# Performance work log

Measured on AMD Instinct MI355X. Metric: run time of the kernel, lower is better.

The kernel has to match this reference:

```python
import jax, jax.numpy as jnp
import numpy as np

B, N = 2, 8192
D_POINTS, D_MODEL, K = 64, 128, 16


def _lin(key, fi, fo):
    return jax.random.normal(key, (fi, fo), jnp.float32) / np.sqrt(fi)


def setup_inputs() -> dict:
    key = jax.random.key(0)
    ks = jax.random.split(key, 16)
    return {
        "xyz": jax.random.normal(ks[0], (B, N, 3), jnp.float32),
        "normals": jax.random.normal(ks[1], (B, N, 3), jnp.float32),
        "features": jax.random.normal(ks[2], (B, N, D_POINTS), jnp.float32),
        "fc1_w": _lin(ks[3], D_POINTS, D_MODEL), "fc1_b": jnp.zeros((D_MODEL,), jnp.float32),
        "fc2_w": _lin(ks[4], D_MODEL, D_POINTS), "fc2_b": jnp.zeros((D_POINTS,), jnp.float32),
        "gamma_w1": _lin(ks[5], D_MODEL, D_MODEL), "gamma_b1": jnp.zeros((D_MODEL,), jnp.float32),
        "gamma_w2": _lin(ks[6], D_MODEL, D_MODEL), "gamma_b2": jnp.zeros((D_MODEL,), jnp.float32),
        "delta_w1": _lin(ks[7], 3, D_MODEL), "delta_b1": jnp.zeros((D_MODEL,), jnp.float32),
        "delta_w2": _lin(ks[8], D_MODEL, D_MODEL), "delta_b2": jnp.zeros((D_MODEL,), jnp.float32),
        "wq": _lin(ks[9], D_MODEL, D_MODEL),
        "wk": _lin(ks[10], D_MODEL, D_MODEL),
        "wv": _lin(ks[11], D_MODEL, D_MODEL),
    }


def _gather(points, idx):
    # points: (b, n, c), idx: (b, n, k) -> (b, n, k, c)
    b, n, c = points.shape
    k = idx.shape[-1]
    flat = jnp.take_along_axis(points, idx.reshape(b, n * k, 1), axis=1)
    return flat.reshape(b, n, k, c)


def reference(xyz, normals, features, fc1_w, fc1_b, fc2_w, fc2_b,
              gamma_w1, gamma_b1, gamma_w2, gamma_b2,
              delta_w1, delta_b1, delta_w2, delta_b2, wq, wk, wv):
    # pairwise squared distances (b, n, n)
    sq = jnp.sum(xyz * xyz, axis=-1)
    dists = sq[:, :, None] + sq[:, None, :] - 2.0 * jnp.einsum('bnd,bmd->bnm', xyz, xyz)
    _, knn_idx = jax.lax.top_k(-dists, K)  # k smallest distances (includes self)

    knn_xyz = _gather(xyz, knn_idx)                      # (b, n, k, 3)
    x = features @ fc1_w + fc1_b                         # (b, n, d_model)
    q = x @ wq                                           # (b, n, d_model)
    k_nbr = _gather(x @ wk, knn_idx)                     # (b, n, k, d_model)
    v_nbr = _gather(x @ wv, knn_idx)                     # (b, n, k, d_model)

    # positional encoding: fc_delta(rel_pos), ends with ReLU
    rel = xyz[:, :, None, :] - knn_xyz                   # (b, n, k, 3)
    pos_enc = jax.nn.relu(jax.nn.relu(rel @ delta_w1 + delta_b1) @ delta_w2 + delta_b2)

    # vector attention logits: fc_gamma(q - k + pos_enc)
    h = q[:, :, None, :] - k_nbr + pos_enc
    logits = jax.nn.relu(h @ gamma_w1 + gamma_b1) @ gamma_w2 + gamma_b2
    attn = jax.nn.softmax(logits / np.sqrt(D_MODEL), axis=-2)  # softmax over neighbors

    res = jnp.einsum('bnkf,bnkf->bnf', attn, v_nbr + pos_enc)
    res = res @ fc2_w + fc2_b + features
    return res, attn
```

## Files before the change

### kernel.cpp

```cpp
#include <hip/hip_runtime.h>
#include <cstdint>

typedef unsigned long long ull;
typedef __bf16 bf16x8 __attribute__((ext_vector_type(8)));
typedef float f32x4 __attribute__((ext_vector_type(4)));
typedef float f32x2 __attribute__((ext_vector_type(2)));

#define NPTS 8192
#define NB 2
#define KNN 16
#define DM 128
#define PADK 136

__device__ __forceinline__ float sq3f(float x, float y, float z) {
    return __fadd_rn(__fadd_rn(__fmul_rn(x, x), __fmul_rn(y, y)), __fmul_rn(z, z));
}
__device__ __forceinline__ unsigned ford(unsigned u) {
    return (u & 0x80000000u) ? ~u : (u | 0x80000000u);
}
__device__ __forceinline__ float inv_ford(unsigned f) {
    unsigned u = (f & 0x80000000u) ? (f ^ 0x80000000u) : ~f;
    return __uint_as_float(u);
}
__device__ __forceinline__ f32x2 pk_mul(f32x2 a, f32x2 b) {
    f32x2 d;
    asm("v_pk_mul_f32 %0, %1, %2" : "=v"(d) : "v"(a), "v"(b));
    return d;
}
__device__ __forceinline__ f32x2 pk_add(f32x2 a, f32x2 b) {
    f32x2 d;
    asm("v_pk_add_f32 %0, %1, %2" : "=v"(d) : "v"(a), "v"(b));
    return d;
}

__device__ __forceinline__ void knn_body(const float* __restrict__ xyz,
                                         int* __restrict__ idx_out,
                                         char* lds, int bid) {
    float4* xsA = (float4*)lds;
    float4* xsB = (float4*)(lds + 8192);
    const int t = threadIdx.x;
    const int wv = t >> 6, lane = t & 63;
    const int q_id = bid * 4 + wv;
    const int b = q_id >> 13;
    const int i = q_id & (NPTS - 1);
    const float* xb = xyz + (size_t)b * NPTS * 3;
    const float qx = xb[3 * i + 0], qy = xb[3 * i + 1], qz = xb[3 * i + 2];
    const float sqi = sq3f(qx, qy, qz);
    const f32x2 qx2 = {qx, qx}, qy2 = {qy, qy}, qz2 = {qz, qz};
    const f32x2 sqi2 = {sqi, sqi}, ntwo2 = {-2.0f, -2.0f};

    unsigned list_hi = 0xffffffffu, list_lo = 0xffffffffu;
    float thrF = __uint_as_float(0x7f800000u);

#define INSERT(FC, CKLO)                                                                 \
    {                                                                                    \
        unsigned ck_hi = ford(__float_as_uint(FC));                                      \
        unsigned ck_lo = (CKLO);                                                         \
        unsigned ph = __shfl_up(list_hi, 1);                                             \
        unsigned pl = __shfl_up(list_lo, 1);                                             \
        bool lt = (ck_hi < list_hi) || (ck_hi == list_hi && ck_lo < list_lo);            \
        bool ge = (lane == 0) || (ck_hi > ph) || (ck_hi == ph && ck_lo >= pl);           \
        list_hi = lt ? (ge ? ck_hi : ph) : list_hi;                                      \
        list_lo = lt ? (ge ? ck_lo : pl) : list_lo;                                      \
        unsigned th = (unsigned)__builtin_amdgcn_readlane((int)list_hi, 15);             \
        th = (th > 0xff800000u) ? 0xff800000u : th;            \
        thrF = fminf(thrF, inv_ford(th));                                                \
    }

    for (int ch = 0; ch < 8; ++ch) {
        __syncthreads();
#pragma unroll
        for (int e = 0; e < 2; e++) {
            int s = t + e * 256;
            int c0 = ((s >> 6) << 7) + (s & 63);
            int g = ch * 1024 + c0;
            float x0 = xb[3 * g + 0], y0 = xb[3 * g + 1], z0 = xb[3 * g + 2];
            float x1 = xb[3 * (g + 64) + 0], y1 = xb[3 * (g + 64) + 1], z1 = xb[3 * (g + 64) + 2];
            xsA[s] = make_float4(x0, x1, y0, y1);
            xsB[s] = make_float4(z0, z1, sq3f(x0, y0, z0), sq3f(x1, y1, z1));
        }
        __syncthreads();
        for (int m = 0; m < 8; m++) {
            const int s = m * 64 + lane;
            float4 A = xsA[s];
            float4 B = xsB[s];
            f32x2 ax = {A.x, A.y}, ay = {A.z, A.w};
            f32x2 bz = {B.x, B.y}, bs = {B.z, B.w};
            f32x2 p1 = pk_mul(qx2, ax);
            f32x2 p2 = pk_mul(qy2, ay);
            f32x2 p3 = pk_mul(qz2, bz);
            f32x2 s1 = pk_add(p1, p2);
            f32x2 s2 = pk_add(s1, p3);
            f32x2 num = pk_add(sqi2, bs);
            f32x2 tm = pk_mul(ntwo2, s2);
            f32x2 dd = pk_add(num, tm);
            float dA = dd.x, dB = dd.y;
            if (ch == 0 && m == 0) {
                float mn = fminf(dA, dB);
                mn = fminf(mn, __shfl_xor(mn, 1));
                mn = fminf(mn, __shfl_xor(mn, 2));
                float mx = mn;
                mx = fmaxf(mx, __shfl_xor(mx, 4));
                mx = fmaxf(mx, __shfl_xor(mx, 8));
                mx = fmaxf(mx, __shfl_xor(mx, 16));
                mx = fmaxf(mx, __shfl_xor(mx, 32));
                thrF = mx;
            }
            ull balA = __ballot(dA <= thrF);
            ull balB = __ballot(dB <= thrF);
            if ((balA | balB) == 0ull) continue;
            const unsigned jbase = (unsigned)(ch * 1024 + m * 128);
            while (balA) {
                int l = (int)__builtin_ctzll(balA);
                balA &= balA - 1;
                float fc = __uint_as_float(
                    (unsigned)__builtin_amdgcn_readlane(__float_as_int(dA), l));
                if (fc <= thrF) INSERT(fc, jbase + (unsigned)l)
            }
            while (balB) {
                int l = (int)__builtin_ctzll(balB);
                balB &= balB - 1;
                float fc = __uint_as_float(
                    (unsigned)__builtin_amdgcn_readlane(__float_as_int(dB), l));
                if (fc <= thrF) INSERT(fc, jbase + 64u + (unsigned)l)
            }
        }
    }
#undef INSERT
    if (lane < 16)
        idx_out[q_id * 16 + lane] = (int)list_lo;
}

__device__ __forceinline__ void xqkv_body(const float* __restrict__ feats,
                                          const float* __restrict__ fc1_w,
                                          const float* __restrict__ fc1_b,
                                          const __bf16* __restrict__ wqt,
                                          const __bf16* __restrict__ wkt,
                                          const __bf16* __restrict__ wvt,
                                          float* __restrict__ qo,
                                          float* __restrict__ kko,
                                          float* __restrict__ vvo,
                                          char* lds, int bid) {
    float* At = (float*)lds;
    __bf16* Ab = (__bf16*)lds;
    const int t = threadIdx.x;
    const int base = bid * 64;

#pragma unroll
    for (int e = 0; e < 16; e++) {
        int id = t + e * 256;
        int r = id >> 6, c = id & 63;
        At[c * 65 + r] = feats[(size_t)(base + r) * 64 + c];
    }
    __syncthreads();
    const int r0 = (t >> 4) * 4;
    const int c0 = (t & 15) * 8;
    float acc[4][8];
#pragma unroll
    for (int i = 0; i < 4; i++)
#pragma unroll
        for (int j = 0; j < 8; j++) acc[i][j] = fc1_b[c0 + j];
#pragma unroll 4
    for (int kk = 0; kk < 64; ++kk) {
        float a0 = At[kk * 65 + r0 + 0];
        float a1 = At[kk * 65 + r0 + 1];
        float a2 = At[kk * 65 + r0 + 2];
        float a3 = At[kk * 65 + r0 + 3];
        const float4 w0 = *(const float4*)&fc1_w[kk * 128 + c0];
        const float4 w1 = *(const float4*)&fc1_w[kk * 128 + c0 + 4];
        float wj[8] = {w0.x, w0.y, w0.z, w0.w, w1.x, w1.y, w1.z, w1.w};
#pragma unroll
        for (int j = 0; j < 8; j++) {
            acc[0][j] += a0 * wj[j];
            acc[1][j] += a1 * wj[j];
            acc[2][j] += a2 * wj[j];
            acc[3][j] += a3 * wj[j];
        }
    }
    __syncthreads();

#pragma unroll
    for (int i = 0; i < 4; i++)
#pragma unroll
        for (int j = 0; j < 8; j++)
            Ab[(r0 + i) * PADK + c0 + j] = (__bf16)acc[i][j];
    __syncthreads();

    const int lane = t & 63;
    const int lr = lane & 15, lg = lane >> 4;
    const int rbase = (t >> 6) * 16;

#define QGEMM(WPTR, OUT)                                                                   \
    {                                                                                      \
        f32x4 accg[8];                                                                     \
        _Pragma("unroll")                                                                  \
        for (int ct = 0; ct < 8; ct++) accg[ct] = (f32x4){0.f, 0.f, 0.f, 0.f};             \
        _Pragma("unroll")                                                                  \
        for (int kt = 0; kt < 4; kt++) {                                                   \
            const int ko = kt * 32 + 8 * lg;                                               \
            bf16x8 a0 = *(const bf16x8*)&Ab[(rbase + lr) * PADK + ko];                     \
            _Pragma("unroll")                                                              \
            for (int ct = 0; ct < 8; ct++) {                                               \
                bf16x8 bv = *(const bf16x8*)&WPTR[(ct * 16 + lr) * 128 + ko];              \
                accg[ct] = __builtin_amdgcn_mfma_f32_16x16x32_bf16(a0, bv, accg[ct], 0, 0, 0); \
            }                                                                              \
        }                                                                                  \
        _Pragma("unroll")                                                                  \
        for (int ct = 0; ct < 8; ct++)                                                     \
            _Pragma("unroll")                                                              \
            for (int e = 0; e < 4; e++)                                                    \
                OUT[(size_t)(base + rbase + 4 * lg + e) * 128 + ct * 16 + lr] = accg[ct][e]; \
    }

    QGEMM(wqt, qo)
    QGEMM(wkt, kko)
    QGEMM(wvt, vvo)
#undef QGEMM
}

__global__ __launch_bounds__(256, 6) void mega_kernel(const float* __restrict__ xyz,
                                                      int* __restrict__ idxw,
                                                      const float* __restrict__ feats,
                                                      const float* __restrict__ fc1_w,
                                                      const float* __restrict__ fc1_b,
                                                      const __bf16* __restrict__ wqt,
                                                      const __bf16* __restrict__ wkt,
                                                      const __bf16* __restrict__ wvt,
                                                      float* __restrict__ qo,
                                                      float* __restrict__ kko,
                                                      float* __restrict__ vvo) {
    __shared__ __align__(16) char lds[17408];
    if (blockIdx.x < 256)
        xqkv_body(feats, fc1_w, fc1_b, wqt, wkt, wvt, qo, kko, vvo, lds, blockIdx.x);
    else
        knn_body(xyz, idxw, lds, blockIdx.x - 256);
}

__global__ __launch_bounds__(256) void wprep_kernel(const float* __restrict__ d2,
                                                    const float* __restrict__ g1,
                                                    const float* __restrict__ g2,
                                                    const float* __restrict__ wq,
                                                    const float* __restrict__ wk,
                                                    const float* __restrict__ wv,
                                                    __bf16* __restrict__ d2t,
                                                    __bf16* __restrict__ g1t,
                                                    __bf16* __restrict__ g2t,
                                                    __bf16* __restrict__ wqt,
                                                    __bf16* __restrict__ wkt,
                                                    __bf16* __restrict__ wvt) {
    const int bi = blockIdx.x;
    const float* src = (bi == 0) ? d2 : (bi == 1) ? g1 : (bi == 2) ? g2
                     : (bi == 3) ? wq : (bi == 4) ? wk : wv;
    __bf16* dst = (bi == 0) ? d2t : (bi == 1) ? g1t : (bi == 2) ? g2t
                : (bi == 3) ? wqt : (bi == 4) ? wkt : wvt;
#pragma unroll
    for (int e = 0; e < 64; e++) {
        int id = threadIdx.x + e * 256;
        int k = id >> 7, n = id & 127;
        dst[n * 128 + k] = (__bf16)src[id];
    }
}

#define STAGE_W(SRC)                                                                       \
    {                                                                                      \
        _Pragma("unroll")                                                                  \
        for (int e = 0; e < 8; e++) {                                                      \
            int ch = t + e * 256;                                                          \
            int r = ch >> 4, ck = ch & 15;                                                 \
            *(bf16x8*)&Wb[r * PADK + ck * 8] = *(const bf16x8*)&SRC[r * 128 + ck * 8];     \
        }                                                                                  \
    }

#define DO_GEMM(ACC0, ACC1, WPTR)                                                          \
    {                                                                                      \
        _Pragma("unroll")                                                                  \
        for (int kt = 0; kt < 4; kt++) {                                                   \
            const int ko = kt * 32 + 8 * lg;                                               \
            bf16x8 a0 = *(const bf16x8*)&Ab[(rbase + lr) * PADK + ko];                     \
            bf16x8 a1 = *(const bf16x8*)&Ab[(rbase + 16 + lr) * PADK + ko];                \
            _Pragma("unroll")                                                              \
            for (int ct = 0; ct < 8; ct++) {                                               \
                bf16x8 bv = *(const bf16x8*)&WPTR[(ct * 16 + lr) * PADK + ko];             \
                ACC0[ct] = __builtin_amdgcn_mfma_f32_16x16x32_bf16(a0, bv, ACC0[ct], 0, 0, 0); \
                ACC1[ct] = __builtin_amdgcn_mfma_f32_16x16x32_bf16(a1, bv, ACC1[ct], 0, 0, 0); \
            }                                                                              \
        }                                                                                  \
    }

__global__ __launch_bounds__(256, 2) void k345_kernel(const float* __restrict__ xyz,
                                                      const int* __restrict__ idxw,
                                                      const float* __restrict__ q,
                                                      const float* __restrict__ xk,
                                                      const float* __restrict__ xv,
                                                      const float* __restrict__ d1,
                                                      const float* __restrict__ bd1,
                                                      const float* __restrict__ bd2,
                                                      const float* __restrict__ bg1,
                                                      const float* __restrict__ bg2,
                                                      const __bf16* __restrict__ d2t,
                                                      const __bf16* __restrict__ g1t,
                                                      const __bf16* __restrict__ g2t,
                                                      float* __restrict__ attn,
                                                      float* __restrict__ res_pre) {
    __shared__ __bf16 Ab[128 * PADK];
    __shared__ __bf16 Wb[128 * PADK];
    __shared__ float rels[128 * 4];
    __shared__ int jrow[128];
    __shared__ float d1s[3 * 128];
    __shared__ float bd1s[128], bd2s[128], bg1s[128], bg2s[128];

    const int t = threadIdx.x;
    const int wv = t >> 6;
    const int lane = t & 63;
    const int lr = lane & 15, lg = lane >> 4;
    const int R0 = blockIdx.x * 128;
    const int b = R0 >> 17;
    const int rbase = wv * 32;

#pragma unroll
    for (int e = 0; e < 2; e++) { int id = t + e * 256; if (id < 384) d1s[id] = d1[id]; }
    if (t < 128) {
        bd1s[t] = bd1[t]; bd2s[t] = bd2[t]; bg1s[t] = bg1[t]; bg2s[t] = bg2[t];
    } else {
        int r = t - 128;
        int j = idxw[R0 + r];
        jrow[r] = j;
        const float* pn = xyz + (size_t)((R0 + r) >> 4) * 3;
        const float* pj = xyz + (size_t)((b << 13) + j) * 3;
        rels[r * 4 + 0] = pn[0] - pj[0];
        rels[r * 4 + 1] = pn[1] - pj[1];
        rels[r * 4 + 2] = pn[2] - pj[2];
    }
    STAGE_W(d2t)
    __syncthreads();

    {
        const int c = t & 127;
        const float w0 = d1s[c], w1 = d1s[128 + c], w2 = d1s[256 + c], bb = bd1s[c];
#pragma unroll
        for (int e = 0; e < 64; e++) {
            int r = (t >> 7) + e * 2;
            float v = fmaf(rels[r * 4 + 2], w2,
                      fmaf(rels[r * 4 + 1], w1, fmaf(rels[r * 4 + 0], w0, bb)));
            Ab[r * PADK + c] = (__bf16)fmaxf(v, 0.0f);
        }
    }
    __syncthreads();

    f32x4 acc0[8], acc1[8];
#pragma unroll
    for (int ct = 0; ct < 8; ct++) {
        float bb = bd2s[ct * 16 + lr];
        acc0[ct] = (f32x4){bb, bb, bb, bb};
        acc1[ct] = acc0[ct];
    }
    DO_GEMM(acc0, acc1, Wb)
    f32x4 pos0[8], pos1[8];
#pragma unroll
    for (int ct = 0; ct < 8; ct++) {
#pragma unroll
        for (int e = 0; e < 4; e++) {
            pos0[ct][e] = fmaxf(acc0[ct][e], 0.0f);
            pos1[ct][e] = fmaxf(acc1[ct][e], 0.0f);
        }
    }

#pragma unroll
    for (int rt = 0; rt < 2; rt++) {
        const int rloc = rbase + rt * 16 + 4 * lg;
        const size_t qbase = (size_t)((R0 + rloc) >> 4) * 128;
        const int j0 = jrow[rloc + 0], j1 = jrow[rloc + 1];
        const int j2 = jrow[rloc + 2], j3 = jrow[rloc + 3];
        const size_t kb0 = (size_t)((b << 13) + j0) * 128;
        const size_t kb1 = (size_t)((b << 13) + j1) * 128;
        const size_t kb2 = (size_t)((b << 13) + j2) * 128;
        const size_t kb3 = (size_t)((b << 13) + j3) * 128;
        f32x4* posR = rt ? pos1 : pos0;
#pragma unroll
        for (int ct = 0; ct < 8; ct++) {
            const int c = ct * 16 + lr;
            const float qv = q[qbase + c];
            f32x4 p = posR[ct];
            Ab[(rloc + 0) * PADK + c] = (__bf16)(p[0] + qv - xk[kb0 + c]);
            Ab[(rloc + 1) * PADK + c] = (__bf16)(p[1] + qv - xk[kb1 + c]);
            Ab[(rloc + 2) * PADK + c] = (__bf16)(p[2] + qv - xk[kb2 + c]);
            Ab[(rloc + 3) * PADK + c] = (__bf16)(p[3] + qv - xk[kb3 + c]);
        }
    }
    __syncthreads();
    STAGE_W(g1t)
    __syncthreads();

#pragma unroll
    for (int ct = 0; ct < 8; ct++) {
        float bb = bg1s[ct * 16 + lr];
        acc0[ct] = (f32x4){bb, bb, bb, bb};
        acc1[ct] = acc0[ct];
    }
    DO_GEMM(acc0, acc1, Wb)
#pragma unroll
    for (int rt = 0; rt < 2; rt++) {
        const int rloc = rbase + rt * 16 + 4 * lg;
        f32x4* accR = rt ? acc1 : acc0;
#pragma unroll
        for (int ct = 0; ct < 8; ct++) {
            const int c = ct * 16 + lr;
            f32x4 p = accR[ct];
            Ab[(rloc + 0) * PADK + c] = (__bf16)fmaxf(p[0], 0.0f);
            Ab[(rloc + 1) * PADK + c] = (__bf16)fmaxf(p[1], 0.0f);
            Ab[(rloc + 2) * PADK + c] = (__bf16)fmaxf(p[2], 0.0f);
            Ab[(rloc + 3) * PADK + c] = (__bf16)fmaxf(p[3], 0.0f);
        }
    }
    __syncthreads();
    STAGE_W(g2t)
    __syncthreads();

#pragma unroll
    for (int ct = 0; ct < 8; ct++) {
        float bb = bg2s[ct * 16 + lr];
        acc0[ct] = (f32x4){bb, bb, bb, bb};
        acc1[ct] = acc0[ct];
    }
    DO_GEMM(acc0, acc1, Wb)
    const float scale = 0.08838834764831845f;
#pragma unroll
    for (int rt = 0; rt < 2; rt++) {
        const int rloc = rbase + rt * 16 + 4 * lg;
        const int j0 = jrow[rloc + 0], j1 = jrow[rloc + 1];
        const int j2 = jrow[rloc + 2], j3 = jrow[rloc + 3];
        const size_t vb0 = (size_t)((b << 13) + j0) * 128;
        const size_t vb1 = (size_t)((b << 13) + j1) * 128;
        const size_t vb2 = (size_t)((b << 13) + j2) * 128;
        const size_t vb3 = (size_t)((b << 13) + j3) * 128;
        f32x4* accR = rt ? acc1 : acc0;
        f32x4* posR = rt ? pos1 : pos0;
#pragma unroll
        for (int ct = 0; ct < 8; ct++) {
            const int c = ct * 16 + lr;
            f32x4 p = accR[ct];
            float l0 = p[0] * scale, l1 = p[1] * scale, l2 = p[2] * scale, l3 = p[3] * scale;
            float m = fmaxf(fmaxf(l0, l1), fmaxf(l2, l3));
            m = fmaxf(m, __shfl_xor(m, 16));
            m = fmaxf(m, __shfl_xor(m, 32));
            float e0 = __expf(l0 - m), e1 = __expf(l1 - m);
            float e2 = __expf(l2 - m), e3 = __expf(l3 - m);
            float s = (e0 + e1) + (e2 + e3);
            s += __shfl_xor(s, 16);
            s += __shfl_xor(s, 32);
            float inv = 1.0f / s;
            float a0 = e0 * inv, a1 = e1 * inv, a2 = e2 * inv, a3 = e3 * inv;
            size_t ob = (size_t)(R0 + rloc) * 128 + c;
            attn[ob + 0 * 128] = a0;
            attn[ob + 1 * 128] = a1;
            attn[ob + 2 * 128] = a2;
            attn[ob + 3 * 128] = a3;
            f32x4 pp = posR[ct];
            float r = a0 * (xv[vb0 + c] + pp[0])
                    + a1 * (xv[vb1 + c] + pp[1])
                    + a2 * (xv[vb2 + c] + pp[2])
                    + a3 * (xv[vb3 + c] + pp[3]);
            r += __shfl_xor(r, 16);
            r += __shfl_xor(r, 32);
            if (lg == 0)
                res_pre[(size_t)((R0 >> 4) + wv * 2 + rt) * 128 + c] = r;
        }
    }
}

__global__ __launch_bounds__(256, 1) void k6_kernel(const float* __restrict__ res_pre,
                                                    const float* __restrict__ w,
                                                    const float* __restrict__ bias,
                                                    const float* __restrict__ feats,
                                                    float* __restrict__ res_out) {
    __shared__ float At[128 * 65];
    __shared__ __align__(16) float Wt[128 * 64];
    const int t = threadIdx.x;
    const int base = blockIdx.x * 64;
#pragma unroll
    for (int e = 0; e < 32; e++) {
        int id = t + e * 256;
        int r = id >> 7, c = id & 127;
        At[c * 65 + r] = res_pre[(size_t)(base + r) * 128 + c];
    }
#pragma unroll
    for (int e = 0; e < 32; e++) { int id = t + e * 256; Wt[id] = w[id]; }
    __syncthreads();
    const int r0 = (t >> 4) * 4;
    const int c0 = (t & 15) * 4;
    float acc[4][4];
#pragma unroll
    for (int i = 0; i < 4; i++)
#pragma unroll
        for (int j = 0; j < 4; j++) acc[i][j] = bias[c0 + j];
#pragma unroll 4
    for (int kk = 0; kk < 128; ++kk) {
        float a0 = At[kk * 65 + r0 + 0];
        float a1 = At[kk * 65 + r0 + 1];
        float a2 = At[kk * 65 + r0 + 2];
        float a3 = At[kk * 65 + r0 + 3];
        const float4 w0 = *(const float4*)&Wt[kk * 64 + c0];
        float wj[4] = {w0.x, w0.y, w0.z, w0.w};
#pragma unroll
        for (int j = 0; j < 4; j++) {
            acc[0][j] += a0 * wj[j];
            acc[1][j] += a1 * wj[j];
            acc[2][j] += a2 * wj[j];
            acc[3][j] += a3 * wj[j];
        }
    }
#pragma unroll
    for (int i = 0; i < 4; i++)
#pragma unroll
        for (int j = 0; j < 4; j++)
            res_out[(size_t)(base + r0 + i) * 64 + c0 + j] =
                acc[i][j] + feats[(size_t)(base + r0 + i) * 64 + c0 + j];
}

extern "C" void kernel_launch(void* const* d_in, const int* in_sizes, int n_in,
                              void* d_out, int out_size, void* d_ws, size_t ws_size,
                              hipStream_t stream) {
    (void)in_sizes; (void)n_in; (void)out_size; (void)ws_size;
    const float* xyz   = (const float*)d_in[0];
    const float* feats = (const float*)d_in[2];
    const float* fc1_w = (const float*)d_in[3];
    const float* fc1_b = (const float*)d_in[4];
    const float* fc2_w = (const float*)d_in[5];
    const float* fc2_b = (const float*)d_in[6];
    const float* g1    = (const float*)d_in[7];
    const float* bg1   = (const float*)d_in[8];
    const float* g2    = (const float*)d_in[9];
    const float* bg2   = (const float*)d_in[10];
    const float* d1    = (const float*)d_in[11];
    const float* bd1   = (const float*)d_in[12];
    const float* d2    = (const float*)d_in[13];
    const float* bd2   = (const float*)d_in[14];
    const float* wq    = (const float*)d_in[15];
    const float* wk    = (const float*)d_in[16];
    const float* wv    = (const float*)d_in[17];

    int* idxw   = (int*)d_ws;
    float* qbuf = (float*)((char*)d_ws + (1 << 20));
    float* kbuf = qbuf + 2097152;
    float* vbuf = kbuf + 2097152;
    float* rpre = vbuf + 2097152;
    __bf16* d2t = (__bf16*)(rpre + 2097152);
    __bf16* g1t = d2t + 16384;
    __bf16* g2t = g1t + 16384;
    __bf16* wqt = g2t + 16384;
    __bf16* wkt = wqt + 16384;
    __bf16* wvt = wkt + 16384;

    float* res_out = (float*)d_out;
    float* attn    = res_out + 1048576;

    wprep_kernel<<<6, 256, 0, stream>>>(d2, g1, g2, wq, wk, wv,
                                        d2t, g1t, g2t, wqt, wkt, wvt);
    mega_kernel<<<4352, 256, 0, stream>>>(xyz, idxw, feats, fc1_w, fc1_b,
                                          wqt, wkt, wvt, qbuf, kbuf, vbuf);
    k345_kernel<<<2048, 256, 0, stream>>>(xyz, idxw, qbuf, kbuf, vbuf, d1, bd1, bd2, bg1, bg2,
                                          d2t, g1t, g2t, attn, rpre);
    k6_kernel<<<256, 256, 0, stream>>>(rpre, fc2_w, fc2_b, feats, res_out);
}
```

Baseline: 247.9 us.

## Fuse fc2 into attention kernel, read weights from global, interleave knn/qkv blocks

The final fc2 projection kernel is removed. Each attention block now computes its 8 output rows of fc2 plus residual directly from an LDS buffer, which drops the res_pre round trip and one launch. The MFMA GEMMs read bf16 weight fragments straight from global/L2 instead of staging them into a padded LDS buffer. That frees LDS and lets occupancy rise to 3 blocks per CU, at the cost of unpadded global reads. The mega kernel also interleaves one qkv block per 16 knn blocks so the two workloads mix across CUs instead of running in sequence.

```diff
diff --git a/kernel.cpp b/kernel.cpp
--- a/kernel.cpp
+++ b/kernel.cpp
@@ -230,10 +230,12 @@
                                                       float* __restrict__ kko,
                                                       float* __restrict__ vvo) {
     __shared__ __align__(16) char lds[17408];
-    if (blockIdx.x < 256)
-        xqkv_body(feats, fc1_w, fc1_b, wqt, wkt, wvt, qo, kko, vvo, lds, blockIdx.x);
+    const int g = blockIdx.x / 17;
+    const int p = blockIdx.x % 17;
+    if (p == 0)
+        xqkv_body(feats, fc1_w, fc1_b, wqt, wkt, wvt, qo, kko, vvo, lds, g);
     else
-        knn_body(xyz, idxw, lds, blockIdx.x - 256);
+        knn_body(xyz, idxw, lds, g * 16 + (p - 1));
 }
 
 __global__ __launch_bounds__(256) void wprep_kernel(const float* __restrict__ d2,
@@ -261,17 +263,7 @@
     }
 }
 
-#define STAGE_W(SRC)                                                                       \
-    {                                                                                      \
-        _Pragma("unroll")                                                                  \
-        for (int e = 0; e < 8; e++) {                                                      \
-            int ch = t + e * 256;                                                          \
-            int r = ch >> 4, ck = ch & 15;                                                 \
-            *(bf16x8*)&Wb[r * PADK + ck * 8] = *(const bf16x8*)&SRC[r * 128 + ck * 8];     \
-        }                                                                                  \
-    }
-
-#define DO_GEMM(ACC0, ACC1, WPTR)                                                          \
+#define DO_GEMM_G(ACC0, ACC1, WPTR)                                                        \
     {                                                                                      \
         _Pragma("unroll")                                                                  \
         for (int kt = 0; kt < 4; kt++) {                                                   \
@@ -280,14 +272,14 @@
             bf16x8 a1 = *(const bf16x8*)&Ab[(rbase + 16 + lr) * PADK + ko];                \
             _Pragma("unroll")                                                              \
             for (int ct = 0; ct < 8; ct++) {                                               \
-                bf16x8 bv = *(const bf16x8*)&WPTR[(ct * 16 + lr) * PADK + ko];             \
+                bf16x8 bv = *(const bf16x8*)&WPTR[(ct * 16 + lr) * 128 + ko];              \
                 ACC0[ct] = __builtin_amdgcn_mfma_f32_16x16x32_bf16(a0, bv, ACC0[ct], 0, 0, 0); \
                 ACC1[ct] = __builtin_amdgcn_mfma_f32_16x16x32_bf16(a1, bv, ACC1[ct], 0, 0, 0); \
             }                                                                              \
         }                                                                                  \
     }
 
-__global__ __launch_bounds__(256, 2) void k345_kernel(const float* __restrict__ xyz,
+__global__ __launch_bounds__(256, 3) void k345_kernel(const float* __restrict__ xyz,
                                                       const int* __restrict__ idxw,
                                                       const float* __restrict__ q,
                                                       const float* __restrict__ xk,
@@ -300,10 +292,13 @@
                                                       const __bf16* __restrict__ d2t,
                                                       const __bf16* __restrict__ g1t,
                                                       const __bf16* __restrict__ g2t,
+                                                      const float* __restrict__ feats,
+                                                      const float* __restrict__ fc2,
+                                                      const float* __restrict__ fc2_b,
                                                       float* __restrict__ attn,
-                                                      float* __restrict__ res_pre) {
+                                                      float* __restrict__ res_out) {
     __shared__ __bf16 Ab[128 * PADK];
-    __shared__ __bf16 Wb[128 * PADK];
+    __shared__ float rpre_s[8][128];
     __shared__ float rels[128 * 4];
     __shared__ int jrow[128];
     __shared__ float d1s[3 * 128];
@@ -331,7 +326,6 @@
         rels[r * 4 + 1] = pn[1] - pj[1];
         rels[r * 4 + 2] = pn[2] - pj[2];
     }
-    STAGE_W(d2t)
     __syncthreads();
 
     {
@@ -354,7 +348,7 @@
         acc0[ct] = (f32x4){bb, bb, bb, bb};
         acc1[ct] = acc0[ct];
     }
-    DO_GEMM(acc0, acc1, Wb)
+    DO_GEMM_G(acc0, acc1, d2t)
     f32x4 pos0[8], pos1[8];
 #pragma unroll
     for (int ct = 0; ct < 8; ct++) {
@@ -388,8 +382,6 @@
         }
     }
     __syncthreads();
-    STAGE_W(g1t)
-    __syncthreads();
 
 #pragma unroll
     for (int ct = 0; ct < 8; ct++) {
@@ -397,7 +389,8 @@
         acc0[ct] = (f32x4){bb, bb, bb, bb};
         acc1[ct] = acc0[ct];
     }
-    DO_GEMM(acc0, acc1, Wb)
+    DO_GEMM_G(acc0, acc1, g1t)
+    __syncthreads();
 #pragma unroll
     for (int rt = 0; rt < 2; rt++) {
         const int rloc = rbase + rt * 16 + 4 * lg;
@@ -413,8 +406,6 @@
         }
     }
     __syncthreads();
-    STAGE_W(g2t)
-    __syncthreads();
 
 #pragma unroll
     for (int ct = 0; ct < 8; ct++) {
@@ -422,7 +413,7 @@
         acc0[ct] = (f32x4){bb, bb, bb, bb};
         acc1[ct] = acc0[ct];
     }
-    DO_GEMM(acc0, acc1, Wb)
+    DO_GEMM_G(acc0, acc1, g2t)
     const float scale = 0.08838834764831845f;
 #pragma unroll
     for (int rt = 0; rt < 2; rt++) {
@@ -463,58 +454,26 @@
             r += __shfl_xor(r, 16);
             r += __shfl_xor(r, 32);
             if (lg == 0)
-                res_pre[(size_t)((R0 >> 4) + wv * 2 + rt) * 128 + c] = r;
-        }
-    }
-}
-
-__global__ __launch_bounds__(256, 1) void k6_kernel(const float* __restrict__ res_pre,
-                                                    const float* __restrict__ w,
-                                                    const float* __restrict__ bias,
-                                                    const float* __restrict__ feats,
-                                                    float* __restrict__ res_out) {
-    __shared__ float At[128 * 65];
-    __shared__ __align__(16) float Wt[128 * 64];
-    const int t = threadIdx.x;
-    const int base = blockIdx.x * 64;
-#pragma unroll
-    for (int e = 0; e < 32; e++) {
-        int id = t + e * 256;
-        int r = id >> 7, c = id & 127;
-        At[c * 65 + r] = res_pre[(size_t)(base + r) * 128 + c];
-    }
-#pragma unroll
-    for (int e = 0; e < 32; e++) { int id = t + e * 256; Wt[id] = w[id]; }
-    __syncthreads();
-    const int r0 = (t >> 4) * 4;
-    const int c0 = (t & 15) * 4;
-    float acc[4][4];
-#pragma unroll
-    for (int i = 0; i < 4; i++)
-#pragma unroll
-        for (int j = 0; j < 4; j++) acc[i][j] = bias[c0 + j];
-#pragma unroll 4
-    for (int kk = 0; kk < 128; ++kk) {
-        float a0 = At[kk * 65 + r0 + 0];
-        float a1 = At[kk * 65 + r0 + 1];
-        float a2 = At[kk * 65 + r0 + 2];
-        float a3 = At[kk * 65 + r0 + 3];
-        const float4 w0 = *(const float4*)&Wt[kk * 64 + c0];
-        float wj[4] = {w0.x, w0.y, w0.z, w0.w};
-#pragma unroll
-        for (int j = 0; j < 4; j++) {
-            acc[0][j] += a0 * wj[j];
-            acc[1][j] += a1 * wj[j];
-            acc[2][j] += a2 * wj[j];
-            acc[3][j] += a3 * wj[j];
-        }
-    }
-#pragma unroll
-    for (int i = 0; i < 4; i++)
-#pragma unroll
-        for (int j = 0; j < 4; j++)
-            res_out[(size_t)(base + r0 + i) * 64 + c0 + j] =
-                acc[i][j] + feats[(size_t)(base + r0 + i) * 64 + c0 + j];
+                rpre_s[wv * 2 + rt][c] = r;
+        }
+    }
+    __syncthreads();
+
+    {
+        const int row = t >> 5;
+        const int col = (t & 31) * 2;
+        float a0e = fc2_b[col], a1e = fc2_b[col + 1];
+#pragma unroll 8
+        for (int kk = 0; kk < 128; ++kk) {
+            float a = rpre_s[row][kk];
+            const float2 w = *(const float2*)&fc2[kk * 64 + col];
+            a0e = fmaf(a, w.x, a0e);
+            a1e = fmaf(a, w.y, a1e);
+        }
+        const size_t orow = (size_t)(R0 >> 4) + row;
+        res_out[orow * 64 + col]     = a0e + feats[orow * 64 + col];
+        res_out[orow * 64 + col + 1] = a1e + feats[orow * 64 + col + 1];
+    }
 }
 
 extern "C" void kernel_launch(void* const* d_in, const int* in_sizes, int n_in,
@@ -559,6 +518,5 @@
     mega_kernel<<<4352, 256, 0, stream>>>(xyz, idxw, feats, fc1_w, fc1_b,
                                           wqt, wkt, wvt, qbuf, kbuf, vbuf);
     k345_kernel<<<2048, 256, 0, stream>>>(xyz, idxw, qbuf, kbuf, vbuf, d1, bd1, bd2, bg1, bg2,
-                                          d2t, g1t, g2t, attn, rpre);
-    k6_kernel<<<256, 256, 0, stream>>>(rpre, fc2_w, fc2_b, feats, res_out);
-}
+                                          d2t, g1t, g2t, feats, fc2_w, fc2_b, attn, res_out);
+}
```

After: 390.5 us. +57.5%, slower.

## Compute fc1 with bf16 MFMA and interleave xqkv blocks among KNN blocks

Applied to the files above, without the earlier changes.

The fc1 projection, previously a scalar FP32 FMA loop over a transposed LDS tile, now runs as bf16 MFMA using a pre-transposed bf16 fc1 weight produced by an extra block in the weight-prep kernel. The mega kernel's block schedule changes so every 17th block does xqkv work and the rest do KNN. Without this, all xqkv blocks run first and then the KNN blocks, so the interleaving is meant to balance GEMM and KNN load across CUs. The cost is bf16 rounding of features and fc1 weights, plus a larger LDS allocation (26624 bytes) that may lower occupancy for the KNN blocks.

```diff
diff --git a/kernel.cpp b/kernel.cpp
--- a/kernel.cpp
+++ b/kernel.cpp
@@ -11,6 +11,7 @@
 #define KNN 16
 #define DM 128
 #define PADK 136
+#define PADF 72
 
 __device__ __forceinline__ float sq3f(float x, float y, float z) {
     return __fadd_rn(__fadd_rn(__fmul_rn(x, x), __fmul_rn(y, y)), __fmul_rn(z, z));
@@ -132,7 +133,7 @@
 }
 
 __device__ __forceinline__ void xqkv_body(const float* __restrict__ feats,
-                                          const float* __restrict__ fc1_w,
+                                          const __bf16* __restrict__ fc1t,
                                           const float* __restrict__ fc1_b,
                                           const __bf16* __restrict__ wqt,
                                           const __bf16* __restrict__ wkt,
@@ -141,54 +142,46 @@
                                           float* __restrict__ kko,
                                           float* __restrict__ vvo,
                                           char* lds, int bid) {
-    float* At = (float*)lds;
-    __bf16* Ab = (__bf16*)lds;
+    __bf16* Af = (__bf16*)lds;
+    __bf16* Ab = (__bf16*)(lds + 9216);
     const int t = threadIdx.x;
     const int base = bid * 64;
 
 #pragma unroll
-    for (int e = 0; e < 16; e++) {
+    for (int e = 0; e < 4; e++) {
         int id = t + e * 256;
-        int r = id >> 6, c = id & 63;
-        At[c * 65 + r] = feats[(size_t)(base + r) * 64 + c];
-    }
-    __syncthreads();
-    const int r0 = (t >> 4) * 4;
-    const int c0 = (t & 15) * 8;
-    float acc[4][8];
-#pragma unroll
-    for (int i = 0; i < 4; i++)
-#pragma unroll
-        for (int j = 0; j < 8; j++) acc[i][j] = fc1_b[c0 + j];
-#pragma unroll 4
-    for (int kk = 0; kk < 64; ++kk) {
-        float a0 = At[kk * 65 + r0 + 0];
-        float a1 = At[kk * 65 + r0 + 1];
-        float a2 = At[kk * 65 + r0 + 2];
-        float a3 = At[kk * 65 + r0 + 3];
-        const float4 w0 = *(const float4*)&fc1_w[kk * 128 + c0];
-        const float4 w1 = *(const float4*)&fc1_w[kk * 128 + c0 + 4];
-        float wj[8] = {w0.x, w0.y, w0.z, w0.w, w1.x, w1.y, w1.z, w1.w};
-#pragma unroll
-        for (int j = 0; j < 8; j++) {
-            acc[0][j] += a0 * wj[j];
-            acc[1][j] += a1 * wj[j];
-            acc[2][j] += a2 * wj[j];
-            acc[3][j] += a3 * wj[j];
-        }
-    }
-    __syncthreads();
-
-#pragma unroll
-    for (int i = 0; i < 4; i++)
-#pragma unroll
-        for (int j = 0; j < 8; j++)
-            Ab[(r0 + i) * PADK + c0 + j] = (__bf16)acc[i][j];
+        int r = id >> 4, c4 = id & 15;
+        float4 v = *(const float4*)&feats[(size_t)(base + r) * 64 + c4 * 4];
+        __bf16* d = &Af[r * PADF + c4 * 4];
+        d[0] = (__bf16)v.x; d[1] = (__bf16)v.y; d[2] = (__bf16)v.z; d[3] = (__bf16)v.w;
+    }
     __syncthreads();
 
     const int lane = t & 63;
     const int lr = lane & 15, lg = lane >> 4;
-    const int rbase = (t >> 6) * 16;
+    const int rb = (t >> 6) * 16;
+
+    f32x4 xacc[8];
+#pragma unroll
+    for (int ct = 0; ct < 8; ct++) {
+        float bb = fc1_b[ct * 16 + lr];
+        xacc[ct] = (f32x4){bb, bb, bb, bb};
+    }
+#pragma unroll
+    for (int kt = 0; kt < 2; kt++) {
+        const int ko = kt * 32 + 8 * lg;
+        bf16x8 a0 = *(const bf16x8*)&Af[(rb + lr) * PADF + ko];
+#pragma unroll
+        for (int ct = 0; ct < 8; ct++) {
+            bf16x8 bv = *(const bf16x8*)&fc1t[(ct * 16 + lr) * 64 + ko];
+            xacc[ct] = __builtin_amdgcn_mfma_f32_16x16x32_bf16(a0, bv, xacc[ct], 0, 0, 0);
+        }
+    }
+#pragma unroll
+    for (int ct = 0; ct < 8; ct++)
+#pragma unroll
+        for (int e = 0; e < 4; e++)
+            Ab[(rb + 4 * lg + e) * PADK + ct * 16 + lr] = (__bf16)xacc[ct][e];
 
 #define QGEMM(WPTR, OUT)                                                                   \
     {                                                                                      \
@@ -198,7 +191,7 @@
         _Pragma("unroll")                                                                  \
         for (int kt = 0; kt < 4; kt++) {                                                   \
             const int ko = kt * 32 + 8 * lg;                                               \
-            bf16x8 a0 = *(const bf16x8*)&Ab[(rbase + lr) * PADK + ko];                     \
+            bf16x8 a0 = *(const bf16x8*)&Ab[(rb + lr) * PADK + ko];                        \
             _Pragma("unroll")                                                              \
             for (int ct = 0; ct < 8; ct++) {                                               \
                 bf16x8 bv = *(const bf16x8*)&WPTR[(ct * 16 + lr) * 128 + ko];              \
@@ -209,7 +202,7 @@
         for (int ct = 0; ct < 8; ct++)                                                     \
             _Pragma("unroll")                                                              \
             for (int e = 0; e < 4; e++)                                                    \
-                OUT[(size_t)(base + rbase + 4 * lg + e) * 128 + ct * 16 + lr] = accg[ct][e]; \
+                OUT[(size_t)(base + rb + 4 * lg + e) * 128 + ct * 16 + lr] = accg[ct][e];  \
     }
 
     QGEMM(wqt, qo)
@@ -221,7 +214,7 @@
 __global__ __launch_bounds__(256, 6) void mega_kernel(const float* __restrict__ xyz,
                                                       int* __restrict__ idxw,
                                                       const float* __restrict__ feats,
-                                                      const float* __restrict__ fc1_w,
+                                                      const __bf16* __restrict__ fc1t,
                                                       const float* __restrict__ fc1_b,
                                                       const __bf16* __restrict__ wqt,
                                                       const __bf16* __restrict__ wkt,
@@ -229,11 +222,13 @@
                                                       float* __restrict__ qo,
                                                       float* __restrict__ kko,
                                                       float* __restrict__ vvo) {
-    __shared__ __align__(16) char lds[17408];
-    if (blockIdx.x < 256)
-        xqkv_body(feats, fc1_w, fc1_b, wqt, wkt, wvt, qo, kko, vvo, lds, blockIdx.x);
+    __shared__ __align__(16) char lds[26624];
+    const int g = blockIdx.x / 17;
+    const int p = blockIdx.x % 17;
+    if (p == 0)
+        xqkv_body(feats, fc1t, fc1_b, wqt, wkt, wvt, qo, kko, vvo, lds, g);
     else
-        knn_body(xyz, idxw, lds, blockIdx.x - 256);
+        knn_body(xyz, idxw, lds, g * 16 + (p - 1));
 }
 
 __global__ __launch_bounds__(256) void wprep_kernel(const float* __restrict__ d2,
@@ -242,13 +237,24 @@
                                                     const float* __restrict__ wq,
                                                     const float* __restrict__ wk,
                                                     const float* __restrict__ wv,
+                                                    const float* __restrict__ fc1,
                                                     __bf16* __restrict__ d2t,
                                                     __bf16* __restrict__ g1t,
                                                     __bf16* __restrict__ g2t,
                                                     __bf16* __restrict__ wqt,
                                                     __bf16* __restrict__ wkt,
-                                                    __bf16* __restrict__ wvt) {
+                                                    __bf16* __restrict__ wvt,
+                                                    __bf16* __restrict__ fc1t) {
     const int bi = blockIdx.x;
+    if (bi == 6) {
+#pragma unroll
+        for (int e = 0; e < 32; e++) {
+            int id = threadIdx.x + e * 256;
+            int k = id >> 7, n = id & 127;
+            fc1t[n * 64 + k] = (__bf16)fc1[id];
+        }
+        return;
+    }
     const float* src = (bi == 0) ? d2 : (bi == 1) ? g1 : (bi == 2) ? g2
                      : (bi == 3) ? wq : (bi == 4) ? wk : wv;
     __bf16* dst = (bi == 0) ? d2t : (bi == 1) ? g1t : (bi == 2) ? g2t
@@ -550,13 +556,14 @@
     __bf16* wqt = g2t + 16384;
     __bf16* wkt = wqt + 16384;
     __bf16* wvt = wkt + 16384;
+    __bf16* fc1t = wvt + 16384;
 
     float* res_out = (float*)d_out;
     float* attn    = res_out + 1048576;
 
-    wprep_kernel<<<6, 256, 0, stream>>>(d2, g1, g2, wq, wk, wv,
-                                        d2t, g1t, g2t, wqt, wkt, wvt);
-    mega_kernel<<<4352, 256, 0, stream>>>(xyz, idxw, feats, fc1_w, fc1_b,
+    wprep_kernel<<<7, 256, 0, stream>>>(d2, g1, g2, wq, wk, wv, fc1_w,
+                                        d2t, g1t, g2t, wqt, wkt, wvt, fc1t);
+    mega_kernel<<<4352, 256, 0, stream>>>(xyz, idxw, feats, fc1t, fc1_b,
                                           wqt, wkt, wvt, qbuf, kbuf, vbuf);
     k345_kernel<<<2048, 256, 0, stream>>>(xyz, idxw, qbuf, kbuf, vbuf, d1, bd1, bd2, bg1, bg2,
                                           d2t, g1t, g2t, attn, rpre);
```

New measurement: 249.8 us. About the same (+0.8%).
